# Kernel optimization log

Hardware: AMD Instinct MI355X
Metric: run time of the kernel (lower is better)

Reference implementation:

```python
import math
import jax, jax.numpy as jnp
import numpy as np

V, S, D, H, HID, L, B = 32000, 1024, 768, 12, 3072, 4, 2
HD = D // H
EPS = 1e-5
CLAMP = 1e9


def setup_inputs() -> dict:
    key = jax.random.key(0)
    ks = jax.random.split(key, 10)
    std = 0.02
    return {
        "W_emb": jax.random.normal(ks[0], (V, D), jnp.float32) * std,      # tied with lm_head
        "pos_emb": jax.random.normal(ks[1], (S, D), jnp.float32) * std,
        "norm1_g": jnp.ones((L, D), jnp.float32),
        "norm1_b": jnp.zeros((L, D), jnp.float32),
        "qkv_w": jax.random.normal(ks[2], (L, 3 * D, D), jnp.float32) * std,
        "qkv_b": jnp.zeros((L, 3 * D), jnp.float32),
        "proj_w": jax.random.normal(ks[3], (L, D, D), jnp.float32) * std,
        "proj_b": jnp.zeros((L, D), jnp.float32),
        "norm2_g": jnp.ones((L, D), jnp.float32),
        "norm2_b": jnp.zeros((L, D), jnp.float32),
        "ffn_w1": jax.random.normal(ks[4], (L, HID, D), jnp.float32) * std,
        "ffn_b1": jnp.zeros((L, HID), jnp.float32),
        "ffn_w2": jax.random.normal(ks[5], (L, D, HID), jnp.float32) * std,
        "ffn_b2": jnp.zeros((L, D), jnp.float32),
        "fin_g": jnp.ones((D,), jnp.float32),
        "fin_b": jnp.zeros((D,), jnp.float32),
        "input_ids": jax.random.randint(ks[6], (B, S), 0, V, jnp.int64),
    }


def layer_norm(x, g, b):
    mean = jnp.mean(x, axis=-1, keepdims=True)
    var = jnp.mean((x - mean) ** 2, axis=-1, keepdims=True)
    return g * ((x - mean) / jnp.sqrt(var + EPS)) + b


def attention(x, qkv_w, qkv_b, proj_w, proj_b):
    b, s, _ = x.shape
    qkv = x @ qkv_w.T + qkv_b                                  # [B,S,3D]
    qkv = qkv.reshape(b, s, H, 3 * HD).transpose(0, 2, 1, 3)   # [B,H,S,3*HD]
    q, k, v = qkv[..., :HD], qkv[..., HD:2 * HD], qkv[..., 2 * HD:]
    scaled = jnp.einsum("bhqd,bhkd->bhqk", q, k) / math.sqrt(HD)
    mask = jnp.tril(jnp.ones((s, s), bool))
    scaled = jnp.clip(jnp.where(mask, scaled, -jnp.inf), -CLAMP, CLAMP)
    attn = jax.nn.softmax(scaled, axis=-1)
    vals = jnp.einsum("bhqk,bhkd->bhqd", attn, v)
    vals = vals.transpose(0, 2, 1, 3).reshape(b, s, D)
    return vals @ proj_w.T + proj_b


def reference(W_emb, pos_emb, norm1_g, norm1_b, qkv_w, qkv_b, proj_w, proj_b,
              norm2_g, norm2_b, ffn_w1, ffn_b1, ffn_w2, ffn_b2, fin_g, fin_b,
              input_ids):
    x = W_emb[input_ids] * math.sqrt(D)          # [B,S,D]
    x = x + pos_emb[None, :x.shape[1], :]
    for i in range(L):
        h = layer_norm(x, norm1_g[i], norm1_b[i])
        x = x + attention(h, qkv_w[i], qkv_b[i], proj_w[i], proj_b[i])
        h = layer_norm(x, norm2_g[i], norm2_b[i])
        h = jax.nn.gelu(h @ ffn_w1[i].T + ffn_b1[i], approximate=False)
        x = x + h @ ffn_w2[i].T + ffn_b2[i]
    x = layer_norm(x, fin_g, fin_b)
    logits = x @ W_emb.T                         # tied lm_head, no bias
    return logits
```

## Files before the change

kernel.cpp:

```cpp
#include <hip/hip_runtime.h>
#include <hip/hip_bf16.h>
#include <math.h>

typedef __bf16 bf16_t;
typedef __bf16 bf16x8 __attribute__((ext_vector_type(8)));
typedef float f32x4 __attribute__((ext_vector_type(4)));

__device__ __forceinline__ void gload16(const bf16_t* g, bf16_t* l) {
  __builtin_amdgcn_global_load_lds(
      (const __attribute__((address_space(1))) unsigned int*)g,
      (__attribute__((address_space(3))) unsigned int*)l, 16, 0, 0);
}


template<int EPI>
__global__ __launch_bounds__(128, 3) void gemm_bt(
    const bf16_t* __restrict__ A, const bf16_t* __restrict__ W,
    const float* __restrict__ bias,
    bf16_t* __restrict__ obf, float* __restrict__ of32, bf16_t* __restrict__ vt,
    int M, int N, int K, int kLen)
{
  __shared__ bf16_t As[128 * 64];
  __shared__ bf16_t Bs[64 * 64];
  const int tid  = threadIdx.x;
  const int lane = tid & 63;
  const int w    = tid >> 6;
  const long m0 = (long)blockIdx.y * 128;
  const long n0 = (long)blockIdx.x * 64;
  const int k0 = blockIdx.z * kLen;
  const int k1 = k0 + kLen;

  f32x4 acc[4][4] = {};

  const int l7  = lane & 7;
  const int l15 = lane & 15;
  const int hi  = lane >> 4;
  const int rA  = w * 64 + l15;

  for (int kt = k0; kt < k1; kt += 64) {
#pragma unroll
    for (int i = 0; i < 8; ++i) {
      const int cl  = tid + i * 128;
      const int row = cl >> 3;
      const int j   = (cl & 7) ^ (row & 7);
      gload16(A + (m0 + row) * K + kt + (j << 3), As + cl * 8);
    }
#pragma unroll
    for (int i = 0; i < 4; ++i) {
      const int cl  = tid + i * 128;
      const int row = cl >> 3;
      const int j   = (cl & 7) ^ (row & 7);
      gload16(W + (n0 + row) * K + kt + (j << 3), Bs + cl * 8);
    }
    __syncthreads();
#pragma unroll
    for (int kk = 0; kk < 64; kk += 32) {
      const int ck = ((((kk >> 3) + hi) ^ l7) << 3);
      bf16x8 af[4], bfr[4];
#pragma unroll
      for (int m = 0; m < 4; ++m) af[m]  = *(const bf16x8*)(As + (rA + m * 16) * 64 + ck);
#pragma unroll
      for (int n = 0; n < 4; ++n) bfr[n] = *(const bf16x8*)(Bs + (l15 + n * 16) * 64 + ck);
#pragma unroll
      for (int m = 0; m < 4; ++m)
#pragma unroll
        for (int n = 0; n < 4; ++n)
          acc[m][n] = __builtin_amdgcn_mfma_f32_16x16x32_bf16(af[m], bfr[n], acc[m][n], 0, 0, 0);
    }
    __syncthreads();
  }

  const int lr = hi << 2;
#pragma unroll
  for (int n = 0; n < 4; ++n) {
    const long gcol = n0 + n * 16 + l15;
    float bv = 0.f;
    if (EPI == 0 || EPI == 1 || EPI == 5) bv = bias[gcol];
    if (EPI == 4 && k0 == 0)  bv = bias[gcol];
    const int hq = (int)gcol / 192;
    const int c  = (int)gcol - hq * 192;
#pragma unroll
    for (int m = 0; m < 4; ++m) {
      const long grow0 = m0 + w * 64 + m * 16 + lr;
#pragma unroll
      for (int r = 0; r < 4; ++r) {
        float v = acc[m][n][r] + bv;
        const long idx = (grow0 + r) * N + gcol;
        if (EPI == 0 || EPI == 5) {
          obf[idx] = (bf16_t)v;
          if (EPI == 5 && c >= 128) {
            const int row = (int)(grow0 + r);
            const int bb = row >> 10, ss = row & 1023;
            vt[(((long)bb * 12 + hq) * 64 + (c - 128)) * 1024 + ss] = (bf16_t)v;
          }
        } else if (EPI == 1) {
          v = 0.5f * v * (1.0f + erff(v * 0.70710678118654752f));
          obf[idx] = (bf16_t)v;
        } else {
          atomicAdd(&of32[idx], v);
        }
      }
    }
  }
}

__global__ __launch_bounds__(256, 2) void gemm_logits(
    const bf16_t* __restrict__ A, const bf16_t* __restrict__ W,
    float* __restrict__ out)
{
  __shared__ bf16_t As[128 * 64];
  __shared__ bf16_t Bs[128 * 64];
  const int tid  = threadIdx.x;
  const int lane = tid & 63;
  const int w    = tid >> 6;
  const int wr   = w >> 1;
  const int wc   = w & 1;
  const int d    = blockIdx.x;
  const int wk   = (d & 7) * 500 + (d >> 3);
  const long m0  = (long)(wk & 15) * 128;
  const long n0  = (long)(wk >> 4) * 128;
  const int K = 768, N = 32000;

  f32x4 acc[4][4] = {};
  const int l7  = lane & 7;
  const int l15 = lane & 15;
  const int hi  = lane >> 4;
  const int rA  = wr * 64 + l15;
  const int rB  = wc * 64 + l15;

  for (int kt = 0; kt < K; kt += 64) {
#pragma unroll
    for (int i = 0; i < 4; ++i) {
      const int cl  = tid + i * 256;
      const int row = cl >> 3;
      const int j   = (cl & 7) ^ (row & 7);
      gload16(A + (m0 + row) * K + kt + (j << 3), As + cl * 8);
    }
#pragma unroll
    for (int i = 0; i < 4; ++i) {
      const int cl  = tid + i * 256;
      const int row = cl >> 3;
      const int j   = (cl & 7) ^ (row & 7);
      gload16(W + (n0 + row) * K + kt + (j << 3), Bs + cl * 8);
    }
    __syncthreads();
#pragma unroll
    for (int kk = 0; kk < 64; kk += 32) {
      const int ck = ((((kk >> 3) + hi) ^ l7) << 3);
      bf16x8 af[4], bfr[4];
#pragma unroll
      for (int m = 0; m < 4; ++m) af[m]  = *(const bf16x8*)(As + (rA + m * 16) * 64 + ck);
#pragma unroll
      for (int n = 0; n < 4; ++n) bfr[n] = *(const bf16x8*)(Bs + (rB + n * 16) * 64 + ck);
#pragma unroll
      for (int m = 0; m < 4; ++m)
#pragma unroll
        for (int n = 0; n < 4; ++n)
          acc[m][n] = __builtin_amdgcn_mfma_f32_16x16x32_bf16(af[m], bfr[n], acc[m][n], 0, 0, 0);
    }
    __syncthreads();
  }

  const int lr = hi << 2;
#pragma unroll
  for (int n = 0; n < 4; ++n) {
    const long gcol = n0 + wc * 64 + n * 16 + l15;
#pragma unroll
    for (int m = 0; m < 4; ++m) {
      const long grow0 = m0 + wr * 64 + m * 16 + lr;
#pragma unroll
      for (int r = 0; r < 4; ++r)
        __builtin_nontemporal_store(acc[m][n][r], &out[(grow0 + r) * N + gcol]);
    }
  }
}

__global__ __launch_bounds__(256) void attn_kernel(
    const bf16_t* __restrict__ qkv, const bf16_t* __restrict__ vT,
    bf16_t* __restrict__ aout)
{
  __shared__ bf16_t Plds[4][16 * 64];
  const int tid  = threadIdx.x;
  const int lane = tid & 63;
  const int w    = tid >> 6;
  const int wid  = blockIdx.x * 4 + w;
  const int qt   = wid & 63;
  const int bh   = wid >> 6;
  const int b    = bh / 12;
  const int h    = bh % 12;
  const int q0   = qt << 4;

  const bf16_t* base = qkv + (long)b * 1024 * 2304 + h * 192;
  const bf16_t* vtb  = vT + (long)bh * 64 * 1024;
  const int koff  = (lane >> 4) << 3;
  const int l15   = lane & 15;
  const int rbase = (lane >> 4) << 2;

  const bf16x8 qf0 = *(const bf16x8*)(base + (long)(q0 + l15) * 2304 + koff);
  const bf16x8 qf1 = *(const bf16x8*)(base + (long)(q0 + l15) * 2304 + 32 + koff);

  f32x4 acc[4] = {};
  float mrun[4], lrun[4];
#pragma unroll
  for (int r = 0; r < 4; ++r) { mrun[r] = -1e30f; lrun[r] = 0.f; }

  bf16_t* pl = &Plds[w][0];
  const int kbmax = (q0 + 15) >> 6;
  for (int kb = 0; kb <= kbmax; ++kb) {
    const int kv0 = kb << 6;
    const f32x4 z = {0.f, 0.f, 0.f, 0.f};
    f32x4 s[4];
    __builtin_amdgcn_s_setprio(1);
#pragma unroll
    for (int g = 0; g < 4; ++g) {
      const bf16_t* kr = base + 64 + (long)(kv0 + g * 16 + l15) * 2304;
      const bf16x8 ka = *(const bf16x8*)(kr + koff);
      const bf16x8 kb2 = *(const bf16x8*)(kr + 32 + koff);
      s[g] = __builtin_amdgcn_mfma_f32_16x16x32_bf16(qf0, ka, z, 0, 0, 0);
      s[g] = __builtin_amdgcn_mfma_f32_16x16x32_bf16(qf1, kb2, s[g], 0, 0, 0);
    }
    __builtin_amdgcn_s_setprio(0);

#pragma unroll
    for (int r = 0; r < 4; ++r) {
      const int qi = q0 + rbase + r;
      float v[4];
#pragma unroll
      for (int g = 0; g < 4; ++g)
        v[g] = (kv0 + g * 16 + l15 <= qi) ? s[g][r] * 0.125f : -1e9f;
      float mx = fmaxf(fmaxf(v[0], v[1]), fmaxf(v[2], v[3]));
#pragma unroll
      for (int dd = 1; dd < 16; dd <<= 1) mx = fmaxf(mx, __shfl_xor(mx, dd));
      const float mnew = fmaxf(mrun[r], mx);
      const float sc = __expf(mrun[r] - mnew);
      float p[4], sm = 0.f;
#pragma unroll
      for (int g = 0; g < 4; ++g) { p[g] = __expf(v[g] - mnew); sm += p[g]; }
#pragma unroll
      for (int dd = 1; dd < 16; dd <<= 1) sm += __shfl_xor(sm, dd);
      lrun[r] = lrun[r] * sc + sm;
      mrun[r] = mnew;
      acc[0][r] *= sc; acc[1][r] *= sc; acc[2][r] *= sc; acc[3][r] *= sc;
#pragma unroll
      for (int g = 0; g < 4; ++g)
        pl[(rbase + r) * 64 + g * 16 + l15] = (bf16_t)p[g];
    }
    asm volatile("s_waitcnt lgkmcnt(0)" ::: "memory");
    const bf16x8 pf0 = *(const bf16x8*)(pl + l15 * 64 + koff);
    const bf16x8 pf1 = *(const bf16x8*)(pl + l15 * 64 + 32 + koff);
    __builtin_amdgcn_s_setprio(1);
#pragma unroll
    for (int hh = 0; hh < 2; ++hh) {
      const bf16x8 pf = hh ? pf1 : pf0;
      const int sbase = kv0 + hh * 32 + koff;
#pragma unroll
      for (int cb = 0; cb < 4; ++cb) {
        const bf16x8 vf = *(const bf16x8*)(vtb + (long)(cb * 16 + l15) * 1024 + sbase);
        acc[cb] = __builtin_amdgcn_mfma_f32_16x16x32_bf16(pf, vf, acc[cb], 0, 0, 0);
      }
    }
    __builtin_amdgcn_s_setprio(0);
  }

#pragma unroll
  for (int cb = 0; cb < 4; ++cb)
#pragma unroll
    for (int r = 0; r < 4; ++r) {
      const float o = acc[cb][r] / lrun[r];
      aout[(long)(b * 1024 + q0 + rbase + r) * 768 + h * 64 + cb * 16 + l15] = (bf16_t)o;
    }
}

__global__ __launch_bounds__(256) void ln_kernel(
    const float* __restrict__ x, const float* __restrict__ g,
    const float* __restrict__ bta, bf16_t* __restrict__ out)
{
  const int row = blockIdx.x;
  const int tid = threadIdx.x;
  const float* xr = x + (long)row * 768;
  const float v0 = xr[tid], v1 = xr[tid + 256], v2 = xr[tid + 512];
  float s  = v0 + v1 + v2;
  float ss = v0 * v0 + v1 * v1 + v2 * v2;
#pragma unroll
  for (int d = 1; d < 64; d <<= 1) { s += __shfl_xor(s, d); ss += __shfl_xor(ss, d); }
  __shared__ float sh[8];
  const int lane = tid & 63, wv = tid >> 6;
  if (lane == 0) { sh[wv] = s; sh[4 + wv] = ss; }
  __syncthreads();
  s  = sh[0] + sh[1] + sh[2] + sh[3];
  ss = sh[4] + sh[5] + sh[6] + sh[7];
  const float mean = s * (1.0f / 768.0f);
  const float var  = ss * (1.0f / 768.0f) - mean * mean;
  const float inv  = rsqrtf(var + 1e-5f);
  bf16_t* orow = out + (long)row * 768;
  orow[tid]       = (bf16_t)(g[tid]       * ((v0 - mean) * inv) + bta[tid]);
  orow[tid + 256] = (bf16_t)(g[tid + 256] * ((v1 - mean) * inv) + bta[tid + 256]);
  orow[tid + 512] = (bf16_t)(g[tid + 512] * ((v2 - mean) * inv) + bta[tid + 512]);
}

__global__ __launch_bounds__(256) void embed_kernel(
    const int* __restrict__ ids, const float* __restrict__ We,
    const float* __restrict__ pos, float* __restrict__ x)
{
  const int row = blockIdx.x;
  const int tid = threadIdx.x;
  const int s = row & 1023;
  const long id = ids[row];
  const float* wr = We + id * 768;
  const float* pr = pos + (long)s * 768;
  float* xr = x + (long)row * 768;
#pragma unroll
  for (int k = 0; k < 3; ++k) {
    const int c = tid + k * 256;
    xr[c] = wr[c] * 27.712812921102035f + pr[c];
  }
}

__global__ __launch_bounds__(256) void cvt_all_kernel(
    const float* __restrict__ s0, const float* __restrict__ s1,
    const float* __restrict__ s2, const float* __restrict__ s3,
    const float* __restrict__ s4, bf16_t* __restrict__ out)
{
  const int b = blockIdx.x;
  const float* src; long rel, obase;
  if      (b < 3456)  { src = s0; rel = (long)b * 2048;          obase = 0;        }
  else if (b < 4608)  { src = s1; rel = (long)(b - 3456) * 2048; obase = 7077888;  }
  else if (b < 9216)  { src = s2; rel = (long)(b - 4608) * 2048; obase = 9437184;  }
  else if (b < 13824) { src = s3; rel = (long)(b - 9216) * 2048; obase = 18874368; }
  else                { src = s4; rel = (long)(b - 13824) * 2048; obase = 28311552; }
  const long i = rel + (long)threadIdx.x * 8;
  const f32x4 a = *(const f32x4*)(src + i);
  const f32x4 c = *(const f32x4*)(src + i + 4);
  bf16x8 o;
#pragma unroll
  for (int j = 0; j < 4; ++j) { o[j] = (bf16_t)a[j]; o[4 + j] = (bf16_t)c[j]; }
  *(bf16x8*)(out + obase + i) = o;
}

extern "C" void kernel_launch(void* const* d_in, const int* in_sizes, int n_in,
                              void* d_out, int out_size, void* d_ws, size_t ws_size,
                              hipStream_t stream)
{
  const float* W_emb = (const float*)d_in[0];
  const float* pos   = (const float*)d_in[1];
  const float* n1g   = (const float*)d_in[2];
  const float* n1b   = (const float*)d_in[3];
  const float* qkvw  = (const float*)d_in[4];
  const float* qkvb  = (const float*)d_in[5];
  const float* projw = (const float*)d_in[6];
  const float* projb = (const float*)d_in[7];
  const float* n2g   = (const float*)d_in[8];
  const float* n2b   = (const float*)d_in[9];
  const float* f1w   = (const float*)d_in[10];
  const float* f1b   = (const float*)d_in[11];
  const float* f2w   = (const float*)d_in[12];
  const float* f2b   = (const float*)d_in[13];
  const float* fing  = (const float*)d_in[14];
  const float* finb  = (const float*)d_in[15];
  const int*   ids   = (const int*)d_in[16];
  float* out = (float*)d_out;

  char* ws = (char*)d_ws;
  float*  x     = (float*)(ws);
  bf16_t* h     = (bf16_t*)(ws + 6291456);
  bf16_t* qkv   = (bf16_t*)(ws + 9437184);
  bf16_t* attn  = (bf16_t*)(ws + 18874368);
  bf16_t* ffn1o = (bf16_t*)(ws + 22020096);
  bf16_t* Wq    = (bf16_t*)(ws + 34603008);
  bf16_t* Wp    = (bf16_t*)(ws + 48758784);
  bf16_t* W1    = (bf16_t*)(ws + 53477376);
  bf16_t* W2    = (bf16_t*)(ws + 72351744);
  bf16_t* We    = (bf16_t*)(ws + 91226112);
  bf16_t* vT    = (bf16_t*)(ws + 140378112);

  cvt_all_kernel<<<dim3(25824), 256, 0, stream>>>(qkvw, projw, f1w, f2w, W_emb, Wq);

  embed_kernel<<<2048, 256, 0, stream>>>(ids, W_emb, pos, x);

  for (int i = 0; i < 4; ++i) {
    ln_kernel<<<2048, 256, 0, stream>>>(x, n1g + i * 768, n1b + i * 768, h);
    gemm_bt<5><<<dim3(36, 16), 128, 0, stream>>>(
        h, Wq + (long)i * 2304 * 768, qkvb + i * 2304, qkv, nullptr, vT,
        2048, 2304, 768, 768);
    attn_kernel<<<384, 256, 0, stream>>>(qkv, vT, attn);
    gemm_bt<4><<<dim3(12, 16, 2), 128, 0, stream>>>(
        attn, Wp + (long)i * 768 * 768, projb + i * 768, nullptr, x, nullptr,
        2048, 768, 768, 384);
    ln_kernel<<<2048, 256, 0, stream>>>(x, n2g + i * 768, n2b + i * 768, h);
    gemm_bt<1><<<dim3(48, 16), 128, 0, stream>>>(
        h, W1 + (long)i * 3072 * 768, f1b + i * 3072, ffn1o, nullptr, nullptr,
        2048, 3072, 768, 768);
    gemm_bt<4><<<dim3(12, 16, 4), 128, 0, stream>>>(
        ffn1o, W2 + (long)i * 768 * 3072, f2b + i * 768, nullptr, x, nullptr,
        2048, 768, 3072, 768);
  }
  ln_kernel<<<2048, 256, 0, stream>>>(x, fing, finb, h);
  gemm_logits<<<dim3(4000), 256, 0, stream>>>(h, We, out);
}
```

Before: 839.1 us.

## Enlarge GEMM tiles to 128x128 and 256x128, add lazy softmax rescaling

Doubles the N tile of the generic GEMM to 128 and the M tile of the logits GEMM to 256. Each warp now computes an 8x4 MFMA block, which raises operand reuse per LDS load and halves grid sizes. The cost is lower occupancy (launch bounds 3 to 2), a larger register and LDS footprint, and fewer blocks for the small GEMMs. Attention also skips the online-softmax rescale unless the row max grows by more than 8, cutting exp and multiply work.

```diff
diff --git a/kernel.cpp b/kernel.cpp
--- a/kernel.cpp
+++ b/kernel.cpp
@@ -14,28 +14,27 @@
 
 
 template<int EPI>
-__global__ __launch_bounds__(128, 3) void gemm_bt(
+__global__ __launch_bounds__(128, 2) void gemm_bt(
     const bf16_t* __restrict__ A, const bf16_t* __restrict__ W,
     const float* __restrict__ bias,
     bf16_t* __restrict__ obf, float* __restrict__ of32, bf16_t* __restrict__ vt,
     int M, int N, int K, int kLen)
 {
   __shared__ bf16_t As[128 * 64];
-  __shared__ bf16_t Bs[64 * 64];
+  __shared__ bf16_t Bs[128 * 64];
   const int tid  = threadIdx.x;
   const int lane = tid & 63;
   const int w    = tid >> 6;
   const long m0 = (long)blockIdx.y * 128;
-  const long n0 = (long)blockIdx.x * 64;
+  const long n0 = (long)blockIdx.x * 128;
   const int k0 = blockIdx.z * kLen;
   const int k1 = k0 + kLen;
 
-  f32x4 acc[4][4] = {};
+  f32x4 acc[8][4] = {};
 
   const int l7  = lane & 7;
   const int l15 = lane & 15;
   const int hi  = lane >> 4;
-  const int rA  = w * 64 + l15;
 
   for (int kt = k0; kt < k1; kt += 64) {
 #pragma unroll
@@ -46,7 +45,7 @@
       gload16(A + (m0 + row) * K + kt + (j << 3), As + cl * 8);
     }
 #pragma unroll
-    for (int i = 0; i < 4; ++i) {
+    for (int i = 0; i < 8; ++i) {
       const int cl  = tid + i * 128;
       const int row = cl >> 3;
       const int j   = (cl & 7) ^ (row & 7);
@@ -56,13 +55,13 @@
 #pragma unroll
     for (int kk = 0; kk < 64; kk += 32) {
       const int ck = ((((kk >> 3) + hi) ^ l7) << 3);
-      bf16x8 af[4], bfr[4];
-#pragma unroll
-      for (int m = 0; m < 4; ++m) af[m]  = *(const bf16x8*)(As + (rA + m * 16) * 64 + ck);
-#pragma unroll
-      for (int n = 0; n < 4; ++n) bfr[n] = *(const bf16x8*)(Bs + (l15 + n * 16) * 64 + ck);
-#pragma unroll
-      for (int m = 0; m < 4; ++m)
+      bf16x8 af[8], bfr[4];
+#pragma unroll
+      for (int m = 0; m < 8; ++m) af[m]  = *(const bf16x8*)(As + (m * 16 + l15) * 64 + ck);
+#pragma unroll
+      for (int n = 0; n < 4; ++n) bfr[n] = *(const bf16x8*)(Bs + (w * 64 + n * 16 + l15) * 64 + ck);
+#pragma unroll
+      for (int m = 0; m < 8; ++m)
 #pragma unroll
         for (int n = 0; n < 4; ++n)
           acc[m][n] = __builtin_amdgcn_mfma_f32_16x16x32_bf16(af[m], bfr[n], acc[m][n], 0, 0, 0);
@@ -70,18 +69,17 @@
     __syncthreads();
   }
 
-  const int lr = hi << 2;
 #pragma unroll
   for (int n = 0; n < 4; ++n) {
-    const long gcol = n0 + n * 16 + l15;
+    const long gcol = n0 + w * 64 + n * 16 + l15;
     float bv = 0.f;
     if (EPI == 0 || EPI == 1 || EPI == 5) bv = bias[gcol];
     if (EPI == 4 && k0 == 0)  bv = bias[gcol];
     const int hq = (int)gcol / 192;
     const int c  = (int)gcol - hq * 192;
 #pragma unroll
-    for (int m = 0; m < 4; ++m) {
-      const long grow0 = m0 + w * 64 + m * 16 + lr;
+    for (int m = 0; m < 8; ++m) {
+      const long grow0 = m0 + m * 16 + (hi << 2);
 #pragma unroll
       for (int r = 0; r < 4; ++r) {
         float v = acc[m][n][r] + bv;
@@ -108,29 +106,27 @@
     const bf16_t* __restrict__ A, const bf16_t* __restrict__ W,
     float* __restrict__ out)
 {
-  __shared__ bf16_t As[128 * 64];
+  __shared__ bf16_t As[256 * 64];
   __shared__ bf16_t Bs[128 * 64];
   const int tid  = threadIdx.x;
   const int lane = tid & 63;
   const int w    = tid >> 6;
-  const int wr   = w >> 1;
-  const int wc   = w & 1;
+  const int wm   = w >> 1;
+  const int wn   = w & 1;
   const int d    = blockIdx.x;
-  const int wk   = (d & 7) * 500 + (d >> 3);
-  const long m0  = (long)(wk & 15) * 128;
-  const long n0  = (long)(wk >> 4) * 128;
+  const int wk   = (d & 7) * 250 + (d >> 3);
+  const long m0  = (long)(wk & 7) * 256;
+  const long n0  = (long)(wk >> 3) * 128;
   const int K = 768, N = 32000;
 
-  f32x4 acc[4][4] = {};
+  f32x4 acc[8][4] = {};
   const int l7  = lane & 7;
   const int l15 = lane & 15;
   const int hi  = lane >> 4;
-  const int rA  = wr * 64 + l15;
-  const int rB  = wc * 64 + l15;
 
   for (int kt = 0; kt < K; kt += 64) {
 #pragma unroll
-    for (int i = 0; i < 4; ++i) {
+    for (int i = 0; i < 8; ++i) {
       const int cl  = tid + i * 256;
       const int row = cl >> 3;
       const int j   = (cl & 7) ^ (row & 7);
@@ -147,13 +143,15 @@
 #pragma unroll
     for (int kk = 0; kk < 64; kk += 32) {
       const int ck = ((((kk >> 3) + hi) ^ l7) << 3);
-      bf16x8 af[4], bfr[4];
-#pragma unroll
-      for (int m = 0; m < 4; ++m) af[m]  = *(const bf16x8*)(As + (rA + m * 16) * 64 + ck);
-#pragma unroll
-      for (int n = 0; n < 4; ++n) bfr[n] = *(const bf16x8*)(Bs + (rB + n * 16) * 64 + ck);
-#pragma unroll
-      for (int m = 0; m < 4; ++m)
+      bf16x8 af[8], bfr[4];
+#pragma unroll
+      for (int m = 0; m < 8; ++m)
+        af[m]  = *(const bf16x8*)(As + (wm * 128 + m * 16 + l15) * 64 + ck);
+#pragma unroll
+      for (int n = 0; n < 4; ++n)
+        bfr[n] = *(const bf16x8*)(Bs + (wn * 64 + n * 16 + l15) * 64 + ck);
+#pragma unroll
+      for (int m = 0; m < 8; ++m)
 #pragma unroll
         for (int n = 0; n < 4; ++n)
           acc[m][n] = __builtin_amdgcn_mfma_f32_16x16x32_bf16(af[m], bfr[n], acc[m][n], 0, 0, 0);
@@ -161,13 +159,12 @@
     __syncthreads();
   }
 
-  const int lr = hi << 2;
 #pragma unroll
   for (int n = 0; n < 4; ++n) {
-    const long gcol = n0 + wc * 64 + n * 16 + l15;
-#pragma unroll
-    for (int m = 0; m < 4; ++m) {
-      const long grow0 = m0 + wr * 64 + m * 16 + lr;
+    const long gcol = n0 + wn * 64 + n * 16 + l15;
+#pragma unroll
+    for (int m = 0; m < 8; ++m) {
+      const long grow0 = m0 + wm * 128 + m * 16 + (hi << 2);
 #pragma unroll
       for (int r = 0; r < 4; ++r)
         __builtin_nontemporal_store(acc[m][n][r], &out[(grow0 + r) * N + gcol]);
@@ -231,16 +228,18 @@
       float mx = fmaxf(fmaxf(v[0], v[1]), fmaxf(v[2], v[3]));
 #pragma unroll
       for (int dd = 1; dd < 16; dd <<= 1) mx = fmaxf(mx, __shfl_xor(mx, dd));
-      const float mnew = fmaxf(mrun[r], mx);
-      const float sc = __expf(mrun[r] - mnew);
+      if (mx > mrun[r] + 8.f) {
+        const float sc = __expf(mrun[r] - mx);
+        lrun[r] *= sc;
+        acc[0][r] *= sc; acc[1][r] *= sc; acc[2][r] *= sc; acc[3][r] *= sc;
+        mrun[r] = mx;
+      }
       float p[4], sm = 0.f;
 #pragma unroll
-      for (int g = 0; g < 4; ++g) { p[g] = __expf(v[g] - mnew); sm += p[g]; }
+      for (int g = 0; g < 4; ++g) { p[g] = __expf(v[g] - mrun[r]); sm += p[g]; }
 #pragma unroll
       for (int dd = 1; dd < 16; dd <<= 1) sm += __shfl_xor(sm, dd);
-      lrun[r] = lrun[r] * sc + sm;
-      mrun[r] = mnew;
-      acc[0][r] *= sc; acc[1][r] *= sc; acc[2][r] *= sc; acc[3][r] *= sc;
+      lrun[r] += sm;
 #pragma unroll
       for (int g = 0; g < 4; ++g)
         pl[(rbase + r) * 64 + g * 16 + l15] = (bf16_t)p[g];
@@ -379,21 +378,21 @@
 
   for (int i = 0; i < 4; ++i) {
     ln_kernel<<<2048, 256, 0, stream>>>(x, n1g + i * 768, n1b + i * 768, h);
-    gemm_bt<5><<<dim3(36, 16), 128, 0, stream>>>(
+    gemm_bt<5><<<dim3(18, 16), 128, 0, stream>>>(
         h, Wq + (long)i * 2304 * 768, qkvb + i * 2304, qkv, nullptr, vT,
         2048, 2304, 768, 768);
     attn_kernel<<<384, 256, 0, stream>>>(qkv, vT, attn);
-    gemm_bt<4><<<dim3(12, 16, 2), 128, 0, stream>>>(
+    gemm_bt<4><<<dim3(6, 16, 2), 128, 0, stream>>>(
         attn, Wp + (long)i * 768 * 768, projb + i * 768, nullptr, x, nullptr,
         2048, 768, 768, 384);
     ln_kernel<<<2048, 256, 0, stream>>>(x, n2g + i * 768, n2b + i * 768, h);
-    gemm_bt<1><<<dim3(48, 16), 128, 0, stream>>>(
+    gemm_bt<1><<<dim3(24, 16), 128, 0, stream>>>(
         h, W1 + (long)i * 3072 * 768, f1b + i * 3072, ffn1o, nullptr, nullptr,
         2048, 3072, 768, 768);
-    gemm_bt<4><<<dim3(12, 16, 4), 128, 0, stream>>>(
+    gemm_bt<4><<<dim3(6, 16, 4), 128, 0, stream>>>(
         ffn1o, W2 + (long)i * 768 * 3072, f2b + i * 768, nullptr, x, nullptr,
         2048, 768, 3072, 768);
   }
   ln_kernel<<<2048, 256, 0, stream>>>(x, fing, finb, h);
-  gemm_logits<<<dim3(4000), 256, 0, stream>>>(h, We, out);
-}
+  gemm_logits<<<dim3(2000), 256, 0, stream>>>(h, We, out);
+}
```

Result: slower. 950.6 us (+13.3%).

## Transpose MFMA operands for vectorized epilogue stores and add lazy softmax rescaling

Applied to the files above, without the earlier changes.

Swaps the A/B operands of the MFMA in both GEMM kernels so each lane holds four consecutive columns, which lets the epilogue load bias as a float4 and write outputs as packed 4-wide bf16 or fp32 stores instead of scattered scalar stores. In the attention kernel, the online softmax now rescales the accumulator and running sum only when the new max exceeds the old one by more than 8, skipping the per-tile exp and multiplies otherwise. This trades some numerical headroom, since unnormalized probabilities can reach e^8, for fewer ALU ops. The V-transpose scatter and the atomic-add path remain per-element.

```diff
diff --git a/kernel.cpp b/kernel.cpp
--- a/kernel.cpp
+++ b/kernel.cpp
@@ -5,11 +5,16 @@
 typedef __bf16 bf16_t;
 typedef __bf16 bf16x8 __attribute__((ext_vector_type(8)));
 typedef float f32x4 __attribute__((ext_vector_type(4)));
+typedef unsigned short ushort4v __attribute__((ext_vector_type(4)));
 
 __device__ __forceinline__ void gload16(const bf16_t* g, bf16_t* l) {
   __builtin_amdgcn_global_load_lds(
       (const __attribute__((address_space(1))) unsigned int*)g,
       (__attribute__((address_space(3))) unsigned int*)l, 16, 0, 0);
+}
+
+__device__ __forceinline__ unsigned short bfbits(float v) {
+  union { bf16_t b; unsigned short u; } cv; cv.b = (bf16_t)v; return cv.u;
 }
 
 
@@ -65,40 +70,47 @@
       for (int m = 0; m < 4; ++m)
 #pragma unroll
         for (int n = 0; n < 4; ++n)
-          acc[m][n] = __builtin_amdgcn_mfma_f32_16x16x32_bf16(af[m], bfr[n], acc[m][n], 0, 0, 0);
+          acc[m][n] = __builtin_amdgcn_mfma_f32_16x16x32_bf16(bfr[n], af[m], acc[m][n], 0, 0, 0);
     }
     __syncthreads();
   }
 
-  const int lr = hi << 2;
 #pragma unroll
   for (int n = 0; n < 4; ++n) {
-    const long gcol = n0 + n * 16 + l15;
-    float bv = 0.f;
-    if (EPI == 0 || EPI == 1 || EPI == 5) bv = bias[gcol];
-    if (EPI == 4 && k0 == 0)  bv = bias[gcol];
-    const int hq = (int)gcol / 192;
-    const int c  = (int)gcol - hq * 192;
+    const long cb = n0 + n * 16 + (hi << 2);
+    f32x4 b4 = {0.f, 0.f, 0.f, 0.f};
+    if (EPI == 0 || EPI == 1 || EPI == 5 || (EPI == 4 && k0 == 0))
+      b4 = *(const f32x4*)(bias + cb);
+    int hq = 0, ch = 0;
+    if (EPI == 5) { hq = (int)cb / 192; ch = (int)cb - hq * 192; }
 #pragma unroll
     for (int m = 0; m < 4; ++m) {
-      const long grow0 = m0 + w * 64 + m * 16 + lr;
-#pragma unroll
-      for (int r = 0; r < 4; ++r) {
-        float v = acc[m][n][r] + bv;
-        const long idx = (grow0 + r) * N + gcol;
-        if (EPI == 0 || EPI == 5) {
-          obf[idx] = (bf16_t)v;
-          if (EPI == 5 && c >= 128) {
-            const int row = (int)(grow0 + r);
-            const int bb = row >> 10, ss = row & 1023;
-            vt[(((long)bb * 12 + hq) * 64 + (c - 128)) * 1024 + ss] = (bf16_t)v;
-          }
-        } else if (EPI == 1) {
-          v = 0.5f * v * (1.0f + erff(v * 0.70710678118654752f));
-          obf[idx] = (bf16_t)v;
-        } else {
-          atomicAdd(&of32[idx], v);
+      const long grow = m0 + w * 64 + m * 16 + l15;
+      f32x4 v;
+#pragma unroll
+      for (int r = 0; r < 4; ++r) v[r] = acc[m][n][r] + b4[r];
+      if (EPI == 0 || EPI == 5) {
+        ushort4v st;
+#pragma unroll
+        for (int r = 0; r < 4; ++r) st[r] = bfbits(v[r]);
+        *(ushort4v*)(obf + grow * N + cb) = st;
+        if (EPI == 5 && ch >= 128) {
+          const int bb = (int)(grow >> 10), ss = (int)(grow & 1023);
+#pragma unroll
+          for (int r = 0; r < 4; ++r)
+            vt[(((long)bb * 12 + hq) * 64 + (ch - 128 + r)) * 1024 + ss] = (bf16_t)v[r];
         }
+      } else if (EPI == 1) {
+        ushort4v st;
+#pragma unroll
+        for (int r = 0; r < 4; ++r) {
+          const float g = 0.5f * v[r] * (1.0f + erff(v[r] * 0.70710678118654752f));
+          st[r] = bfbits(g);
+        }
+        *(ushort4v*)(obf + grow * N + cb) = st;
+      } else {
+#pragma unroll
+        for (int r = 0; r < 4; ++r) atomicAdd(&of32[grow * N + cb + r], v[r]);
       }
     }
   }
@@ -156,21 +168,22 @@
       for (int m = 0; m < 4; ++m)
 #pragma unroll
         for (int n = 0; n < 4; ++n)
-          acc[m][n] = __builtin_amdgcn_mfma_f32_16x16x32_bf16(af[m], bfr[n], acc[m][n], 0, 0, 0);
+          acc[m][n] = __builtin_amdgcn_mfma_f32_16x16x32_bf16(bfr[n], af[m], acc[m][n], 0, 0, 0);
     }
     __syncthreads();
   }
 
-  const int lr = hi << 2;
-#pragma unroll
-  for (int n = 0; n < 4; ++n) {
-    const long gcol = n0 + wc * 64 + n * 16 + l15;
-#pragma unroll
-    for (int m = 0; m < 4; ++m) {
-      const long grow0 = m0 + wr * 64 + m * 16 + lr;
-#pragma unroll
-      for (int r = 0; r < 4; ++r)
-        __builtin_nontemporal_store(acc[m][n][r], &out[(grow0 + r) * N + gcol]);
+#pragma unroll
+  for (int m = 0; m < 4; ++m) {
+    const long grow = m0 + wr * 64 + m * 16 + l15;
+#pragma unroll
+    for (int n = 0; n < 4; ++n) {
+      const long cb = n0 + wc * 64 + n * 16 + (hi << 2);
+      float* p = out + grow * N + cb;
+      __builtin_nontemporal_store(acc[m][n][0], p);
+      __builtin_nontemporal_store(acc[m][n][1], p + 1);
+      __builtin_nontemporal_store(acc[m][n][2], p + 2);
+      __builtin_nontemporal_store(acc[m][n][3], p + 3);
     }
   }
 }
@@ -231,16 +244,18 @@
       float mx = fmaxf(fmaxf(v[0], v[1]), fmaxf(v[2], v[3]));
 #pragma unroll
       for (int dd = 1; dd < 16; dd <<= 1) mx = fmaxf(mx, __shfl_xor(mx, dd));
-      const float mnew = fmaxf(mrun[r], mx);
-      const float sc = __expf(mrun[r] - mnew);
+      if (mx > mrun[r] + 8.f) {
+        const float sc = __expf(mrun[r] - mx);
+        lrun[r] *= sc;
+        acc[0][r] *= sc; acc[1][r] *= sc; acc[2][r] *= sc; acc[3][r] *= sc;
+        mrun[r] = mx;
+      }
       float p[4], sm = 0.f;
 #pragma unroll
-      for (int g = 0; g < 4; ++g) { p[g] = __expf(v[g] - mnew); sm += p[g]; }
+      for (int g = 0; g < 4; ++g) { p[g] = __expf(v[g] - mrun[r]); sm += p[g]; }
 #pragma unroll
       for (int dd = 1; dd < 16; dd <<= 1) sm += __shfl_xor(sm, dd);
-      lrun[r] = lrun[r] * sc + sm;
-      mrun[r] = mnew;
-      acc[0][r] *= sc; acc[1][r] *= sc; acc[2][r] *= sc; acc[3][r] *= sc;
+      lrun[r] += sm;
 #pragma unroll
       for (int g = 0; g < 4; ++g)
         pl[(rbase + r) * 64 + g * 16 + l15] = (bf16_t)p[g];
```

Measured after the change: 1.174 ms. +39.9%, slower.

## Replace split-K atomics with partial buffers fused into layernorm; lazy softmax rescale

Applied to the files above, without the earlier changes.

The split-K projection and FFN2 GEMMs no longer atomically add into the residual. Each K-split now writes its own fp32 partial tile, and a new layernorm kernel sums the residual plus both partials, writes the residual back, and normalizes. FFN2 drops from 4 to 2 K-splits. Attention now rescales the running max only when the new max exceeds the old one by more than 8, which skips most rescale multiplies but lets probabilities reach up to e^8 before normalization.

```diff
diff --git a/kernel.cpp b/kernel.cpp
--- a/kernel.cpp
+++ b/kernel.cpp
@@ -76,7 +76,7 @@
     const long gcol = n0 + n * 16 + l15;
     float bv = 0.f;
     if (EPI == 0 || EPI == 1 || EPI == 5) bv = bias[gcol];
-    if (EPI == 4 && k0 == 0)  bv = bias[gcol];
+    if (EPI == 6 && k0 == 0)  bv = bias[gcol];
     const int hq = (int)gcol / 192;
     const int c  = (int)gcol - hq * 192;
 #pragma unroll
@@ -97,7 +97,7 @@
           v = 0.5f * v * (1.0f + erff(v * 0.70710678118654752f));
           obf[idx] = (bf16_t)v;
         } else {
-          atomicAdd(&of32[idx], v);
+          of32[(long)blockIdx.z * ((long)M * N) + idx] = v;
         }
       }
     }
@@ -231,16 +231,18 @@
       float mx = fmaxf(fmaxf(v[0], v[1]), fmaxf(v[2], v[3]));
 #pragma unroll
       for (int dd = 1; dd < 16; dd <<= 1) mx = fmaxf(mx, __shfl_xor(mx, dd));
-      const float mnew = fmaxf(mrun[r], mx);
-      const float sc = __expf(mrun[r] - mnew);
+      if (mx > mrun[r] + 8.f) {
+        const float sc = __expf(mrun[r] - mx);
+        lrun[r] *= sc;
+        acc[0][r] *= sc; acc[1][r] *= sc; acc[2][r] *= sc; acc[3][r] *= sc;
+        mrun[r] = mx;
+      }
       float p[4], sm = 0.f;
 #pragma unroll
-      for (int g = 0; g < 4; ++g) { p[g] = __expf(v[g] - mnew); sm += p[g]; }
+      for (int g = 0; g < 4; ++g) { p[g] = __expf(v[g] - mrun[r]); sm += p[g]; }
 #pragma unroll
       for (int dd = 1; dd < 16; dd <<= 1) sm += __shfl_xor(sm, dd);
-      lrun[r] = lrun[r] * sc + sm;
-      mrun[r] = mnew;
-      acc[0][r] *= sc; acc[1][r] *= sc; acc[2][r] *= sc; acc[3][r] *= sc;
+      lrun[r] += sm;
 #pragma unroll
       for (int g = 0; g < 4; ++g)
         pl[(rbase + r) * 64 + g * 16 + l15] = (bf16_t)p[g];
@@ -296,6 +298,45 @@
   orow[tid]       = (bf16_t)(g[tid]       * ((v0 - mean) * inv) + bta[tid]);
   orow[tid + 256] = (bf16_t)(g[tid + 256] * ((v1 - mean) * inv) + bta[tid + 256]);
   orow[tid + 512] = (bf16_t)(g[tid + 512] * ((v2 - mean) * inv) + bta[tid + 512]);
+}
+
+__global__ __launch_bounds__(256) void ln_fuse2(
+    float* __restrict__ x, const float* __restrict__ dl,
+    const float* __restrict__ g, const float* __restrict__ bta,
+    bf16_t* __restrict__ out)
+{
+  const int row = blockIdx.x;
+  const int tid = threadIdx.x;
+  float* xr = x + (long)row * 768;
+  const float* d0 = dl + (long)row * 768;
+  const float* d1 = dl + 1572864 + (long)row * 768;
+  float v[3];
+#pragma unroll
+  for (int k = 0; k < 3; ++k) {
+    const int c = tid + k * 256;
+    const float t = xr[c] + d0[c] + d1[c];
+    v[k] = t;
+    xr[c] = t;
+  }
+  float s  = v[0] + v[1] + v[2];
+  float ss = v[0] * v[0] + v[1] * v[1] + v[2] * v[2];
+#pragma unroll
+  for (int d = 1; d < 64; d <<= 1) { s += __shfl_xor(s, d); ss += __shfl_xor(ss, d); }
+  __shared__ float sh[8];
+  const int lane = tid & 63, wv = tid >> 6;
+  if (lane == 0) { sh[wv] = s; sh[4 + wv] = ss; }
+  __syncthreads();
+  s  = sh[0] + sh[1] + sh[2] + sh[3];
+  ss = sh[4] + sh[5] + sh[6] + sh[7];
+  const float mean = s * (1.0f / 768.0f);
+  const float var  = ss * (1.0f / 768.0f) - mean * mean;
+  const float inv  = rsqrtf(var + 1e-5f);
+  bf16_t* orow = out + (long)row * 768;
+#pragma unroll
+  for (int k = 0; k < 3; ++k) {
+    const int c = tid + k * 256;
+    orow[c] = (bf16_t)(g[c] * ((v[k] - mean) * inv) + bta[c]);
+  }
 }
 
 __global__ __launch_bounds__(256) void embed_kernel(
@@ -372,28 +413,32 @@
   bf16_t* W2    = (bf16_t*)(ws + 72351744);
   bf16_t* We    = (bf16_t*)(ws + 91226112);
   bf16_t* vT    = (bf16_t*)(ws + 140378112);
+  float*  dpart = (float*)(ws + 143523840);
 
   cvt_all_kernel<<<dim3(25824), 256, 0, stream>>>(qkvw, projw, f1w, f2w, W_emb, Wq);
 
   embed_kernel<<<2048, 256, 0, stream>>>(ids, W_emb, pos, x);
 
   for (int i = 0; i < 4; ++i) {
-    ln_kernel<<<2048, 256, 0, stream>>>(x, n1g + i * 768, n1b + i * 768, h);
+    if (i == 0)
+      ln_kernel<<<2048, 256, 0, stream>>>(x, n1g, n1b, h);
+    else
+      ln_fuse2<<<2048, 256, 0, stream>>>(x, dpart, n1g + i * 768, n1b + i * 768, h);
     gemm_bt<5><<<dim3(36, 16), 128, 0, stream>>>(
         h, Wq + (long)i * 2304 * 768, qkvb + i * 2304, qkv, nullptr, vT,
         2048, 2304, 768, 768);
     attn_kernel<<<384, 256, 0, stream>>>(qkv, vT, attn);
-    gemm_bt<4><<<dim3(12, 16, 2), 128, 0, stream>>>(
-        attn, Wp + (long)i * 768 * 768, projb + i * 768, nullptr, x, nullptr,
+    gemm_bt<6><<<dim3(12, 16, 2), 128, 0, stream>>>(
+        attn, Wp + (long)i * 768 * 768, projb + i * 768, nullptr, dpart, nullptr,
         2048, 768, 768, 384);
-    ln_kernel<<<2048, 256, 0, stream>>>(x, n2g + i * 768, n2b + i * 768, h);
+    ln_fuse2<<<2048, 256, 0, stream>>>(x, dpart, n2g + i * 768, n2b + i * 768, h);
     gemm_bt<1><<<dim3(48, 16), 128, 0, stream>>>(
         h, W1 + (long)i * 3072 * 768, f1b + i * 3072, ffn1o, nullptr, nullptr,
         2048, 3072, 768, 768);
-    gemm_bt<4><<<dim3(12, 16, 4), 128, 0, stream>>>(
-        ffn1o, W2 + (long)i * 768 * 3072, f2b + i * 768, nullptr, x, nullptr,
-        2048, 768, 3072, 768);
-  }
-  ln_kernel<<<2048, 256, 0, stream>>>(x, fing, finb, h);
+    gemm_bt<6><<<dim3(12, 16, 2), 128, 0, stream>>>(
+        ffn1o, W2 + (long)i * 768 * 3072, f2b + i * 768, nullptr, dpart, nullptr,
+        2048, 768, 3072, 1536);
+  }
+  ln_fuse2<<<2048, 256, 0, stream>>>(x, dpart, fing, finb, h);
   gemm_logits<<<dim3(4000), 256, 0, stream>>>(h, We, out);
 }
```

New measurement: 808.2 us. 3.7% less time.
